# Kernel tuning notes

Measured on AMD Instinct MI355X. Metric: run time of the kernel, lower is better.

The kernel has to match this reference:

```python
import jax, jax.numpy as jnp
import numpy as np

L, B = 64, 7          # n_layers, n_bit_options
EPS = 0.02            # sinkhorn entropic regularizer
ITERS = 200           # sinkhorn iterations
TINY = 1e-40


def setup_inputs() -> dict:
    key = jax.random.key(0)
    k1, k2, k3, k4 = jax.random.split(key, 4)
    theta = jax.random.normal(k1, (L, B), dtype=jnp.float32)
    phi = jax.random.normal(k2, (B,), dtype=jnp.float32)
    # layer sizes (param counts), positive; matches layer_sizes buffer usage
    n = jax.random.uniform(k3, (L,), dtype=jnp.float32, minval=4096.0, maxval=262144.0)
    sens = jax.random.uniform(k4, (L,), dtype=jnp.float32)
    sens = sens / sens.sum()  # update_sensitivity normalizes to a distribution
    bits = jnp.arange(2, 2 + B, dtype=jnp.float32)
    err = 2.0 ** (-2.0 * bits)  # quantization error per bitwidth
    return {"theta": theta, "phi": phi, "n": n, "sens": sens, "err": err}


def reference(theta, phi, n, sens, err):
    # DiffAllocator.compute_P
    a = n / n.sum()                         # row marginal (buffer 'a')
    b = jax.nn.softmax(phi)                 # col marginal b()
    C = (n * sens)[:, None] * err[None, :]  # build_cost: [L,B]
    K = -(C - theta) / EPS                  # log-kernel
    log_a = jnp.log(a + TINY)
    log_b = jnp.log(b + TINY)
    f0 = jnp.zeros((L,), dtype=theta.dtype)
    g0 = jnp.zeros((B,), dtype=theta.dtype)

    def step(carry, _):
        f, g = carry
        f = log_a - jax.scipy.special.logsumexp(K + g[None, :], axis=1)
        g = log_b - jax.scipy.special.logsumexp(K + f[:, None], axis=0)
        return (f, g), None

    (f, g), _ = jax.lax.scan(step, (f0, g0), None, length=ITERS)
    P = jnp.exp(K + f[:, None] + g[None, :])
    return P / (P.sum() + TINY)
```

## Files before the change

### kernel.cpp

```cpp
#include <hip/hip_runtime.h>
#include <math.h>

#define NB 7
#define EPS_ 0.02f
#define ITERS1_ 120
#define ITERS2_ 80
#define TINY_ 1e-40f
#define LOG2E_ 1.4426950408889634f
#define LN2_   0.6931471805599453f

__device__ __forceinline__ float exp2_hw(float x) {
#if __has_builtin(__builtin_amdgcn_exp2f)
    return __builtin_amdgcn_exp2f(x);
#else
    return __expf(x * LN2_);
#endif
}
__device__ __forceinline__ float log2_hw(float x) {
#if __has_builtin(__builtin_amdgcn_logf)
    return __builtin_amdgcn_logf(x);
#else
    return __logf(x) * LOG2E_;
#endif
}
__device__ __forceinline__ float rcp_hw(float x) {
#if __has_builtin(__builtin_amdgcn_rcpf)
    return __builtin_amdgcn_rcpf(x);
#else
    return 1.0f / x;
#endif
}
__device__ __forceinline__ float ldexp_hw(float x, int e) {
#if __has_builtin(__builtin_amdgcn_ldexpf)
    return __builtin_amdgcn_ldexpf(x, e);
#else
    float r; asm("v_ldexp_f32 %0, %1, %2" : "=v"(r) : "v"(x), "v"(e)); return r;
#endif
}
__device__ __forceinline__ float frexp_mant_hw(float x) {
#if __has_builtin(__builtin_amdgcn_frexp_mantf)
    return __builtin_amdgcn_frexp_mantf(x);
#else
    float r; asm("v_frexp_mant_f32 %0, %1" : "=v"(r) : "v"(x)); return r;
#endif
}
__device__ __forceinline__ int frexp_exp_hw(float x) {
#if __has_builtin(__builtin_amdgcn_frexp_expf)
    return __builtin_amdgcn_frexp_expf(x);
#else
    int r; asm("v_frexp_exp_i32_f32 %0, %1" : "=v"(r) : "v"(x)); return r;
#endif
}

template <int CTRL>
__device__ __forceinline__ float dpp_ident(float identity, float x) {
    return __int_as_float(__builtin_amdgcn_update_dpp(
        __float_as_int(identity), __float_as_int(x), CTRL, 0xF, 0xF, false));
}
__device__ __forceinline__ float readlane63(float x) {
    return __int_as_float(__builtin_amdgcn_readlane(__float_as_int(x), 63));
}
__device__ __forceinline__ float wave_sum_bcast(float s) {
    s += dpp_ident<0x111>(0.f, s);
    s += dpp_ident<0x112>(0.f, s);
    s += dpp_ident<0x114>(0.f, s);
    s += dpp_ident<0x118>(0.f, s);
    s += dpp_ident<0x142>(0.f, s);
    s += dpp_ident<0x143>(0.f, s);
    return readlane63(s);
}

#define WAVE_MAXI7(v0,v1,v2,v3,v4,v5,v6, m0,m1,m2,m3,m4,m5,m6)               \
  {                                                                           \
    int r0,r1,r2,r3,r4,r5,r6;                                                 \
    asm("v_max_i32_dpp %0, %14, %14 row_shr:1 row_mask:0xf bank_mask:0xf\n\t" \
        "v_max_i32_dpp %1, %15, %15 row_shr:1 row_mask:0xf bank_mask:0xf\n\t" \
        "v_max_i32_dpp %2, %16, %16 row_shr:1 row_mask:0xf bank_mask:0xf\n\t" \
        "v_max_i32_dpp %3, %17, %17 row_shr:1 row_mask:0xf bank_mask:0xf\n\t" \
        "v_max_i32_dpp %4, %18, %18 row_shr:1 row_mask:0xf bank_mask:0xf\n\t" \
        "v_max_i32_dpp %5, %19, %19 row_shr:1 row_mask:0xf bank_mask:0xf\n\t" \
        "v_max_i32_dpp %6, %20, %20 row_shr:1 row_mask:0xf bank_mask:0xf\n\t" \
        "v_max_i32_dpp %0, %0, %0 row_shr:2 row_mask:0xf bank_mask:0xf\n\t"   \
        "v_max_i32_dpp %1, %1, %1 row_shr:2 row_mask:0xf bank_mask:0xf\n\t"   \
        "v_max_i32_dpp %2, %2, %2 row_shr:2 row_mask:0xf bank_mask:0xf\n\t"   \
        "v_max_i32_dpp %3, %3, %3 row_shr:2 row_mask:0xf bank_mask:0xf\n\t"   \
        "v_max_i32_dpp %4, %4, %4 row_shr:2 row_mask:0xf bank_mask:0xf\n\t"   \
        "v_max_i32_dpp %5, %5, %5 row_shr:2 row_mask:0xf bank_mask:0xf\n\t"   \
        "v_max_i32_dpp %6, %6, %6 row_shr:2 row_mask:0xf bank_mask:0xf\n\t"   \
        "v_max_i32_dpp %0, %0, %0 row_shr:4 row_mask:0xf bank_mask:0xf\n\t"   \
        "v_max_i32_dpp %1, %1, %1 row_shr:4 row_mask:0xf bank_mask:0xf\n\t"   \
        "v_max_i32_dpp %2, %2, %2 row_shr:4 row_mask:0xf bank_mask:0xf\n\t"   \
        "v_max_i32_dpp %3, %3, %3 row_shr:4 row_mask:0xf bank_mask:0xf\n\t"   \
        "v_max_i32_dpp %4, %4, %4 row_shr:4 row_mask:0xf bank_mask:0xf\n\t"   \
        "v_max_i32_dpp %5, %5, %5 row_shr:4 row_mask:0xf bank_mask:0xf\n\t"   \
        "v_max_i32_dpp %6, %6, %6 row_shr:4 row_mask:0xf bank_mask:0xf\n\t"   \
        "v_max_i32_dpp %0, %0, %0 row_shr:8 row_mask:0xf bank_mask:0xf\n\t"   \
        "v_max_i32_dpp %1, %1, %1 row_shr:8 row_mask:0xf bank_mask:0xf\n\t"   \
        "v_max_i32_dpp %2, %2, %2 row_shr:8 row_mask:0xf bank_mask:0xf\n\t"   \
        "v_max_i32_dpp %3, %3, %3 row_shr:8 row_mask:0xf bank_mask:0xf\n\t"   \
        "v_max_i32_dpp %4, %4, %4 row_shr:8 row_mask:0xf bank_mask:0xf\n\t"   \
        "v_max_i32_dpp %5, %5, %5 row_shr:8 row_mask:0xf bank_mask:0xf\n\t"   \
        "v_max_i32_dpp %6, %6, %6 row_shr:8 row_mask:0xf bank_mask:0xf\n\t"   \
        "v_max_i32_dpp %0, %0, %0 row_bcast:15 row_mask:0xa bank_mask:0xf\n\t"\
        "v_max_i32_dpp %1, %1, %1 row_bcast:15 row_mask:0xa bank_mask:0xf\n\t"\
        "v_max_i32_dpp %2, %2, %2 row_bcast:15 row_mask:0xa bank_mask:0xf\n\t"\
        "v_max_i32_dpp %3, %3, %3 row_bcast:15 row_mask:0xa bank_mask:0xf\n\t"\
        "v_max_i32_dpp %4, %4, %4 row_bcast:15 row_mask:0xa bank_mask:0xf\n\t"\
        "v_max_i32_dpp %5, %5, %5 row_bcast:15 row_mask:0xa bank_mask:0xf\n\t"\
        "v_max_i32_dpp %6, %6, %6 row_bcast:15 row_mask:0xa bank_mask:0xf\n\t"\
        "v_max_i32_dpp %0, %0, %0 row_bcast:31 row_mask:0xc bank_mask:0xf\n\t"\
        "v_max_i32_dpp %1, %1, %1 row_bcast:31 row_mask:0xc bank_mask:0xf\n\t"\
        "v_max_i32_dpp %2, %2, %2 row_bcast:31 row_mask:0xc bank_mask:0xf\n\t"\
        "v_max_i32_dpp %3, %3, %3 row_bcast:31 row_mask:0xc bank_mask:0xf\n\t"\
        "v_max_i32_dpp %4, %4, %4 row_bcast:31 row_mask:0xc bank_mask:0xf\n\t"\
        "v_max_i32_dpp %5, %5, %5 row_bcast:31 row_mask:0xc bank_mask:0xf\n\t"\
        "v_max_i32_dpp %6, %6, %6 row_bcast:31 row_mask:0xc bank_mask:0xf\n\t"\
        "v_readlane_b32 %7, %0, 63\n\t"                                       \
        "v_readlane_b32 %8, %1, 63\n\t"                                       \
        "v_readlane_b32 %9, %2, 63\n\t"                                       \
        "v_readlane_b32 %10, %3, 63\n\t"                                      \
        "v_readlane_b32 %11, %4, 63\n\t"                                      \
        "v_readlane_b32 %12, %5, 63\n\t"                                      \
        "v_readlane_b32 %13, %6, 63\n\t"                                      \
        "s_nop 1"                                                             \
        : "=&v"(r0), "=&v"(r1), "=&v"(r2), "=&v"(r3),                         \
          "=&v"(r4), "=&v"(r5), "=&v"(r6),                                    \
          "=s"(m0), "=s"(m1), "=s"(m2), "=s"(m3),                             \
          "=s"(m4), "=s"(m5), "=s"(m6)                                        \
        : "v"(v0), "v"(v1), "v"(v2), "v"(v3), "v"(v4), "v"(v5), "v"(v6));     \
  }

#define WAVE_SUM7(e0,e1,e2,e3,e4,e5,e6, s0_,s1_,s2_,s3_,s4_,s5_,s6_)          \
    asm("s_nop 1\n\t"                                                         \
        "v_add_f32_dpp %0, %0, %0 row_shr:1 row_mask:0xf bank_mask:0xf\n\t"   \
        "v_add_f32_dpp %1, %1, %1 row_shr:1 row_mask:0xf bank_mask:0xf\n\t"   \
        "v_add_f32_dpp %2, %2, %2 row_shr:1 row_mask:0xf bank_mask:0xf\n\t"   \
        "v_add_f32_dpp %3, %3, %3 row_shr:1 row_mask:0xf bank_mask:0xf\n\t"   \
        "v_add_f32_dpp %4, %4, %4 row_shr:1 row_mask:0xf bank_mask:0xf\n\t"   \
        "v_add_f32_dpp %5, %5, %5 row_shr:1 row_mask:0xf bank_mask:0xf\n\t"   \
        "v_add_f32_dpp %6, %6, %6 row_shr:1 row_mask:0xf bank_mask:0xf\n\t"   \
        "v_add_f32_dpp %0, %0, %0 row_shr:2 row_mask:0xf bank_mask:0xf\n\t"   \
        "v_add_f32_dpp %1, %1, %1 row_shr:2 row_mask:0xf bank_mask:0xf\n\t"   \
        "v_add_f32_dpp %2, %2, %2 row_shr:2 row_mask:0xf bank_mask:0xf\n\t"   \
        "v_add_f32_dpp %3, %3, %3 row_shr:2 row_mask:0xf bank_mask:0xf\n\t"   \
        "v_add_f32_dpp %4, %4, %4 row_shr:2 row_mask:0xf bank_mask:0xf\n\t"   \
        "v_add_f32_dpp %5, %5, %5 row_shr:2 row_mask:0xf bank_mask:0xf\n\t"   \
        "v_add_f32_dpp %6, %6, %6 row_shr:2 row_mask:0xf bank_mask:0xf\n\t"   \
        "v_add_f32_dpp %0, %0, %0 row_shr:4 row_mask:0xf bank_mask:0xf\n\t"   \
        "v_add_f32_dpp %1, %1, %1 row_shr:4 row_mask:0xf bank_mask:0xf\n\t"   \
        "v_add_f32_dpp %2, %2, %2 row_shr:4 row_mask:0xf bank_mask:0xf\n\t"   \
        "v_add_f32_dpp %3, %3, %3 row_shr:4 row_mask:0xf bank_mask:0xf\n\t"   \
        "v_add_f32_dpp %4, %4, %4 row_shr:4 row_mask:0xf bank_mask:0xf\n\t"   \
        "v_add_f32_dpp %5, %5, %5 row_shr:4 row_mask:0xf bank_mask:0xf\n\t"   \
        "v_add_f32_dpp %6, %6, %6 row_shr:4 row_mask:0xf bank_mask:0xf\n\t"   \
        "v_add_f32_dpp %0, %0, %0 row_shr:8 row_mask:0xf bank_mask:0xf\n\t"   \
        "v_add_f32_dpp %1, %1, %1 row_shr:8 row_mask:0xf bank_mask:0xf\n\t"   \
        "v_add_f32_dpp %2, %2, %2 row_shr:8 row_mask:0xf bank_mask:0xf\n\t"   \
        "v_add_f32_dpp %3, %3, %3 row_shr:8 row_mask:0xf bank_mask:0xf\n\t"   \
        "v_add_f32_dpp %4, %4, %4 row_shr:8 row_mask:0xf bank_mask:0xf\n\t"   \
        "v_add_f32_dpp %5, %5, %5 row_shr:8 row_mask:0xf bank_mask:0xf\n\t"   \
        "v_add_f32_dpp %6, %6, %6 row_shr:8 row_mask:0xf bank_mask:0xf\n\t"   \
        "v_add_f32_dpp %0, %0, %0 row_bcast:15 row_mask:0xa bank_mask:0xf\n\t"\
        "v_add_f32_dpp %1, %1, %1 row_bcast:15 row_mask:0xa bank_mask:0xf\n\t"\
        "v_add_f32_dpp %2, %2, %2 row_bcast:15 row_mask:0xa bank_mask:0xf\n\t"\
        "v_add_f32_dpp %3, %3, %3 row_bcast:15 row_mask:0xa bank_mask:0xf\n\t"\
        "v_add_f32_dpp %4, %4, %4 row_bcast:15 row_mask:0xa bank_mask:0xf\n\t"\
        "v_add_f32_dpp %5, %5, %5 row_bcast:15 row_mask:0xa bank_mask:0xf\n\t"\
        "v_add_f32_dpp %6, %6, %6 row_bcast:15 row_mask:0xa bank_mask:0xf\n\t"\
        "v_add_f32_dpp %0, %0, %0 row_bcast:31 row_mask:0xc bank_mask:0xf\n\t"\
        "v_add_f32_dpp %1, %1, %1 row_bcast:31 row_mask:0xc bank_mask:0xf\n\t"\
        "v_add_f32_dpp %2, %2, %2 row_bcast:31 row_mask:0xc bank_mask:0xf\n\t"\
        "v_add_f32_dpp %3, %3, %3 row_bcast:31 row_mask:0xc bank_mask:0xf\n\t"\
        "v_add_f32_dpp %4, %4, %4 row_bcast:31 row_mask:0xc bank_mask:0xf\n\t"\
        "v_add_f32_dpp %5, %5, %5 row_bcast:31 row_mask:0xc bank_mask:0xf\n\t"\
        "v_add_f32_dpp %6, %6, %6 row_bcast:31 row_mask:0xc bank_mask:0xf\n\t"\
        "v_readlane_b32 %7, %0, 63\n\t"                                       \
        "v_readlane_b32 %8, %1, 63\n\t"                                       \
        "v_readlane_b32 %9, %2, 63\n\t"                                       \
        "v_readlane_b32 %10, %3, 63\n\t"                                      \
        "v_readlane_b32 %11, %4, 63\n\t"                                      \
        "v_readlane_b32 %12, %5, 63\n\t"                                      \
        "v_readlane_b32 %13, %6, 63\n\t"                                      \
        "s_nop 1"                                                             \
        : "+v"(e0), "+v"(e1), "+v"(e2), "+v"(e3),                             \
          "+v"(e4), "+v"(e5), "+v"(e6),                                       \
          "=s"(s0_), "=s"(s1_), "=s"(s2_), "=s"(s3_),                         \
          "=s"(s4_), "=s"(s5_), "=s"(s6_))

#define WAVE_SUM7_SRC(w0,w1,w2,w3,w4,w5,w6, s0_,s1_,s2_,s3_,s4_,s5_,s6_)     \
  {                                                                           \
    float r0,r1,r2,r3,r4,r5,r6;                                               \
    asm("s_nop 1\n\t"                                                         \
        "v_add_f32_dpp %0, %14, %14 row_shr:1 row_mask:0xf bank_mask:0xf\n\t" \
        "v_add_f32_dpp %1, %15, %15 row_shr:1 row_mask:0xf bank_mask:0xf\n\t" \
        "v_add_f32_dpp %2, %16, %16 row_shr:1 row_mask:0xf bank_mask:0xf\n\t" \
        "v_add_f32_dpp %3, %17, %17 row_shr:1 row_mask:0xf bank_mask:0xf\n\t" \
        "v_add_f32_dpp %4, %18, %18 row_shr:1 row_mask:0xf bank_mask:0xf\n\t" \
        "v_add_f32_dpp %5, %19, %19 row_shr:1 row_mask:0xf bank_mask:0xf\n\t" \
        "v_add_f32_dpp %6, %20, %20 row_shr:1 row_mask:0xf bank_mask:0xf\n\t" \
        "v_add_f32_dpp %0, %0, %0 row_shr:2 row_mask:0xf bank_mask:0xf\n\t"   \
        "v_add_f32_dpp %1, %1, %1 row_shr:2 row_mask:0xf bank_mask:0xf\n\t"   \
        "v_add_f32_dpp %2, %2, %2 row_shr:2 row_mask:0xf bank_mask:0xf\n\t"   \
        "v_add_f32_dpp %3, %3, %3 row_shr:2 row_mask:0xf bank_mask:0xf\n\t"   \
        "v_add_f32_dpp %4, %4, %4 row_shr:2 row_mask:0xf bank_mask:0xf\n\t"   \
        "v_add_f32_dpp %5, %5, %5 row_shr:2 row_mask:0xf bank_mask:0xf\n\t"   \
        "v_add_f32_dpp %6, %6, %6 row_shr:2 row_mask:0xf bank_mask:0xf\n\t"   \
        "v_add_f32_dpp %0, %0, %0 row_shr:4 row_mask:0xf bank_mask:0xf\n\t"   \
        "v_add_f32_dpp %1, %1, %1 row_shr:4 row_mask:0xf bank_mask:0xf\n\t"   \
        "v_add_f32_dpp %2, %2, %2 row_shr:4 row_mask:0xf bank_mask:0xf\n\t"   \
        "v_add_f32_dpp %3, %3, %3 row_shr:4 row_mask:0xf bank_mask:0xf\n\t"   \
        "v_add_f32_dpp %4, %4, %4 row_shr:4 row_mask:0xf bank_mask:0xf\n\t"   \
        "v_add_f32_dpp %5, %5, %5 row_shr:4 row_mask:0xf bank_mask:0xf\n\t"   \
        "v_add_f32_dpp %6, %6, %6 row_shr:4 row_mask:0xf bank_mask:0xf\n\t"   \
        "v_add_f32_dpp %0, %0, %0 row_shr:8 row_mask:0xf bank_mask:0xf\n\t"   \
        "v_add_f32_dpp %1, %1, %1 row_shr:8 row_mask:0xf bank_mask:0xf\n\t"   \
        "v_add_f32_dpp %2, %2, %2 row_shr:8 row_mask:0xf bank_mask:0xf\n\t"   \
        "v_add_f32_dpp %3, %3, %3 row_shr:8 row_mask:0xf bank_mask:0xf\n\t"   \
        "v_add_f32_dpp %4, %4, %4 row_shr:8 row_mask:0xf bank_mask:0xf\n\t"   \
        "v_add_f32_dpp %5, %5, %5 row_shr:8 row_mask:0xf bank_mask:0xf\n\t"   \
        "v_add_f32_dpp %6, %6, %6 row_shr:8 row_mask:0xf bank_mask:0xf\n\t"   \
        "v_add_f32_dpp %0, %0, %0 row_bcast:15 row_mask:0xa bank_mask:0xf\n\t"\
        "v_add_f32_dpp %1, %1, %1 row_bcast:15 row_mask:0xa bank_mask:0xf\n\t"\
        "v_add_f32_dpp %2, %2, %2 row_bcast:15 row_mask:0xa bank_mask:0xf\n\t"\
        "v_add_f32_dpp %3, %3, %3 row_bcast:15 row_mask:0xa bank_mask:0xf\n\t"\
        "v_add_f32_dpp %4, %4, %4 row_bcast:15 row_mask:0xa bank_mask:0xf\n\t"\
        "v_add_f32_dpp %5, %5, %5 row_bcast:15 row_mask:0xa bank_mask:0xf\n\t"\
        "v_add_f32_dpp %6, %6, %6 row_bcast:15 row_mask:0xa bank_mask:0xf\n\t"\
        "v_add_f32_dpp %0, %0, %0 row_bcast:31 row_mask:0xc bank_mask:0xf\n\t"\
        "v_add_f32_dpp %1, %1, %1 row_bcast:31 row_mask:0xc bank_mask:0xf\n\t"\
        "v_add_f32_dpp %2, %2, %2 row_bcast:31 row_mask:0xc bank_mask:0xf\n\t"\
        "v_add_f32_dpp %3, %3, %3 row_bcast:31 row_mask:0xc bank_mask:0xf\n\t"\
        "v_add_f32_dpp %4, %4, %4 row_bcast:31 row_mask:0xc bank_mask:0xf\n\t"\
        "v_add_f32_dpp %5, %5, %5 row_bcast:31 row_mask:0xc bank_mask:0xf\n\t"\
        "v_add_f32_dpp %6, %6, %6 row_bcast:31 row_mask:0xc bank_mask:0xf\n\t"\
        "v_readlane_b32 %7, %0, 63\n\t"                                       \
        "v_readlane_b32 %8, %1, 63\n\t"                                       \
        "v_readlane_b32 %9, %2, 63\n\t"                                       \
        "v_readlane_b32 %10, %3, 63\n\t"                                      \
        "v_readlane_b32 %11, %4, 63\n\t"                                      \
        "v_readlane_b32 %12, %5, 63\n\t"                                      \
        "v_readlane_b32 %13, %6, 63\n\t"                                      \
        "s_nop 1"                                                             \
        : "=&v"(r0), "=&v"(r1), "=&v"(r2), "=&v"(r3),                         \
          "=&v"(r4), "=&v"(r5), "=&v"(r6),                                    \
          "=s"(s0_), "=s"(s1_), "=s"(s2_), "=s"(s3_),                         \
          "=s"(s4_), "=s"(s5_), "=s"(s6_)                                     \
        : "v"(w0), "v"(w1), "v"(w2), "v"(w3), "v"(w4), "v"(w5), "v"(w6));     \
  }

__global__ __launch_bounds__(64) void sinkhorn_kernel(
    const float* __restrict__ theta,
    const float* __restrict__ phi,
    const float* __restrict__ n,
    const float* __restrict__ sens,
    const float* __restrict__ err,
    float* __restrict__ out)
{
    const int lane = threadIdx.x;

    const float ni = n[lane];
    const float si = sens[lane];

    const float kscale = LOG2E_ / EPS_;
    float K2[NB];
    #pragma unroll
    for (int j = 0; j < NB; ++j)
        K2[j] = (theta[lane * NB + j] - ni * si * err[j]) * kscale;

    const float nsum   = wave_sum_bcast(ni);
    const float aT     = ni / nsum + TINY_;
    const float log_a2 = log2_hw(aT);

    float t2v[NB];
    #pragma unroll
    for (int j = 0; j < NB; ++j) t2v[j] = phi[j] * LOG2E_;
    float pmax = t2v[0];
    #pragma unroll
    for (int j = 1; j < NB; ++j) pmax = fmaxf(pmax, t2v[j]);
    float psum = 0.f;
    #pragma unroll
    for (int j = 0; j < NB; ++j) psum += exp2_hw(t2v[j] - pmax);
    const float lps = log2_hw(psum);
    float bT[NB], cb[NB];
    #pragma unroll
    for (int j = 0; j < NB; ++j) {
        bT[j]     = exp2_hw(t2v[j] - pmax - lps) + TINY_;
        const float log_b2 = log2_hw(bT[j]);
        cb[j]     = log_b2 - log_a2;
    }
    float b2c[NB], ibc[NB];
    #pragma unroll
    for (int j = 0; j < NB; ++j) {
        b2c[j] = exp2_hw(cb[j]);
        ibc[j] = exp2_hw(-cb[j]);
    }

    float Mm[NB]; int iE[NB];
    #pragma unroll
    for (int j = 0; j < NB; ++j) {
        const float y  = K2[j] - log_a2;
        const float yi = rintf(y);
        iE[j] = (int)yi;
        Mm[j] = exp2_hw(y - yi);
    }

    int XcS0 = 0, XcS1 = 0, XcS2 = 0, XcS3 = 0, XcS4 = 0, XcS5 = 0, XcS6 = 0;
    const unsigned SLO = 0x17800000u, SHI = 0x67800000u;

    for (int it = 0; it < ITERS1_; ++it) {
        const int X = max(max(max(iE[0], iE[1]), max(iE[2], iE[3])),
                          max(max(iE[4], iE[5]), iE[6]));
        const int xe0 = iE[0]-X, xe1 = iE[1]-X, xe2 = iE[2]-X, xe3 = iE[3]-X,
                  xe4 = iE[4]-X, xe5 = iE[5]-X, xe6 = iE[6]-X;
        const float f0 = ldexp_hw(Mm[0], xe0), f1 = ldexp_hw(Mm[1], xe1),
                    f2 = ldexp_hw(Mm[2], xe2), f3 = ldexp_hw(Mm[3], xe3),
                    f4 = ldexp_hw(Mm[4], xe4), f5 = ldexp_hw(Mm[5], xe5),
                    f6 = ldexp_hw(Mm[6], xe6);
        const float s  = ((f0 + f1) + (f2 + f3)) + ((f4 + f5) + f6);
        const float rs = rcp_hw(s);

        const float g0 = (Mm[0]*ibc[0])*rs, g1 = (Mm[1]*ibc[1])*rs,
                    g2 = (Mm[2]*ibc[2])*rs, g3 = (Mm[3]*ibc[3])*rs,
                    g4 = (Mm[4]*ibc[4])*rs, g5 = (Mm[5]*ibc[5])*rs,
                    g6 = (Mm[6]*ibc[6])*rs;

        int d0 = xe0-XcS0, d1 = xe1-XcS1, d2 = xe2-XcS2, d3 = xe3-XcS3,
            d4 = xe4-XcS4, d5 = xe5-XcS5, d6 = xe6-XcS6;
        float h0 = ldexp_hw(g0, d0), h1 = ldexp_hw(g1, d1),
              h2 = ldexp_hw(g2, d2), h3 = ldexp_hw(g3, d3),
              h4 = ldexp_hw(g4, d4), h5 = ldexp_hw(g5, d5),
              h6 = ldexp_hw(g6, d6);

        float ss0, ss1, ss2, ss3, ss4, ss5, ss6;
        WAVE_SUM7(h0, h1, h2, h3, h4, h5, h6,
                  ss0, ss1, ss2, ss3, ss4, ss5, ss6);

        const unsigned u0 = __float_as_uint(ss0), u1 = __float_as_uint(ss1),
                       u2 = __float_as_uint(ss2), u3 = __float_as_uint(ss3),
                       u4 = __float_as_uint(ss4), u5 = __float_as_uint(ss5),
                       u6 = __float_as_uint(ss6);
        const unsigned umin = min(min(min(u0, u1), min(u2, u3)),
                                  min(min(u4, u5), u6));
        const unsigned umax = max(max(max(u0, u1), max(u2, u3)),
                                  max(max(u4, u5), u6));
        if (umin < SLO || umax > SHI) {
            int C0, C1, C2, C3, C4, C5, C6;
            WAVE_MAXI7(xe0, xe1, xe2, xe3, xe4, xe5, xe6,
                       C0, C1, C2, C3, C4, C5, C6);
            d0 = xe0-C0; d1 = xe1-C1; d2 = xe2-C2; d3 = xe3-C3;
            d4 = xe4-C4; d5 = xe5-C5; d6 = xe6-C6;
            h0 = ldexp_hw(g0, d0); h1 = ldexp_hw(g1, d1);
            h2 = ldexp_hw(g2, d2); h3 = ldexp_hw(g3, d3);
            h4 = ldexp_hw(g4, d4); h5 = ldexp_hw(g5, d5);
            h6 = ldexp_hw(g6, d6);
            WAVE_SUM7(h0, h1, h2, h3, h4, h5, h6,
                      ss0, ss1, ss2, ss3, ss4, ss5, ss6);
            XcS0 = C0; XcS1 = C1; XcS2 = C2; XcS3 = C3;
            XcS4 = C4; XcS5 = C5; XcS6 = C6;
        }

        const float r0 = rcp_hw(ss0), r1 = rcp_hw(ss1), r2 = rcp_hw(ss2),
                    r3 = rcp_hw(ss3), r4 = rcp_hw(ss4), r5 = rcp_hw(ss5),
                    r6 = rcp_hw(ss6);
        const float w0 = (g0*r0)*b2c[0], w1 = (g1*r1)*b2c[1],
                    w2 = (g2*r2)*b2c[2], w3 = (g3*r3)*b2c[3],
                    w4 = (g4*r4)*b2c[4], w5 = (g5*r5)*b2c[5],
                    w6 = (g6*r6)*b2c[6];
        Mm[0] = frexp_mant_hw(w0); iE[0] = frexp_exp_hw(w0) + d0;
        Mm[1] = frexp_mant_hw(w1); iE[1] = frexp_exp_hw(w1) + d1;
        Mm[2] = frexp_mant_hw(w2); iE[2] = frexp_exp_hw(w2) + d2;
        Mm[3] = frexp_mant_hw(w3); iE[3] = frexp_exp_hw(w3) + d3;
        Mm[4] = frexp_mant_hw(w4); iE[4] = frexp_exp_hw(w4) + d4;
        Mm[5] = frexp_mant_hw(w5); iE[5] = frexp_exp_hw(w5) + d5;
        Mm[6] = frexp_mant_hw(w6); iE[6] = frexp_exp_hw(w6) + d6;
    }

    float U[NB], B[NB];
    #pragma unroll
    for (int j = 0; j < NB; ++j) {
        U[j] = ldexp_hw(Mm[j] * ibc[j], iE[j]);
        B[j] = b2c[j];
    }

    for (int it = 0; it < ITERS2_; ++it) {
        float p0 = U[0] * B[0], p1 = U[1] * B[1], p2 = U[2] * B[2],
              p3 = U[3] * B[3], p4 = U[4] * B[4], p5 = U[5] * B[5],
              p6 = U[6] * B[6];
        const float s = ((p0 + p1) + (p2 + p3)) + ((p4 + p5) + p6);
        const float rs = rcp_hw(s);
        float w0 = U[0] * rs, w1 = U[1] * rs, w2 = U[2] * rs,
              w3 = U[3] * rs, w4 = U[4] * rs, w5 = U[5] * rs,
              w6 = U[6] * rs;

        float ss0, ss1, ss2, ss3, ss4, ss5, ss6;
        WAVE_SUM7_SRC(w0, w1, w2, w3, w4, w5, w6,
                      ss0, ss1, ss2, ss3, ss4, ss5, ss6);

        const float r0 = rcp_hw(ss0);
        const float r1 = rcp_hw(ss1);
        const float r2 = rcp_hw(ss2);
        const float r3 = rcp_hw(ss3);
        const float r4 = rcp_hw(ss4);
        const float r5 = rcp_hw(ss5);
        const float r6 = rcp_hw(ss6);
        U[0] = w0 * r0; U[1] = w1 * r1; U[2] = w2 * r2; U[3] = w3 * r3;
        U[4] = w4 * r4; U[5] = w5 * r5; U[6] = w6 * r6;
    }

    float pr[NB];
    float rowsum = 0.f;
    #pragma unroll
    for (int j = 0; j < NB; ++j) {
        pr[j] = U[j] * bT[j];
        rowsum += pr[j];
    }
    const float total = wave_sum_bcast(rowsum);
    const float inv = 1.0f / (total + TINY_);
    #pragma unroll
    for (int j = 0; j < NB; ++j)
        out[lane * NB + j] = pr[j] * inv;
}

extern "C" void kernel_launch(void* const* d_in, const int* in_sizes, int n_in,
                              void* d_out, int out_size, void* d_ws, size_t ws_size,
                              hipStream_t stream) {
    const float* theta = (const float*)d_in[0];
    const float* phi   = (const float*)d_in[1];
    const float* n     = (const float*)d_in[2];
    const float* sens  = (const float*)d_in[3];
    const float* err   = (const float*)d_in[4];
    float* out = (float*)d_out;

    sinkhorn_kernel<<<1, 64, 0, stream>>>(theta, phi, n, sens, err, out);
}
```

Before: 113.8 us.

## Add frozen-exponent fast path for early Sinkhorn phase iterations

Phase 1 of the Sinkhorn loop used to renormalise exponents with frexp and ldexp on every iteration. It now does that only every PERIOD_ iterations, after an initial FULLN_ full iterations. In between it freezes a per-row and per-column power-of-two frame (RA/CA) and runs plain float multiplies, with wave-wide range checks that drop back to the full path on overflow or underflow risk. This removes the ldexp and frexp work from most iterations, but adds ballot and branch overhead plus possible retries, and it relies on the frozen frame staying within range.

```diff
diff --git a/kernel.cpp b/kernel.cpp
--- a/kernel.cpp
+++ b/kernel.cpp
@@ -5,6 +5,8 @@
 #define EPS_ 0.02f
 #define ITERS1_ 120
 #define ITERS2_ 80
+#define FULLN_  16
+#define PERIOD_ 16
 #define TINY_ 1e-40f
 #define LOG2E_ 1.4426950408889634f
 #define LN2_   0.6931471805599453f
@@ -50,6 +52,15 @@
 #else
     int r; asm("v_frexp_exp_i32_f32 %0, %1" : "=v"(r) : "v"(x)); return r;
 #endif
+}
+__device__ __forceinline__ float mant_of(float w) {
+    return __int_as_float((__float_as_int(w) & 0x007fffff) | 0x3f800000);
+}
+__device__ __forceinline__ int exp_of(float w) {
+    return ((__float_as_int(w) >> 23) & 0xff) - 127;
+}
+__device__ __forceinline__ float exp2i_nonpos(int e) {
+    return (e >= -126) ? __int_as_float((e + 127) << 23) : 0.0f;
 }
 
 template <int CTRL>
@@ -295,94 +306,165 @@
         ibc[j] = exp2_hw(-cb[j]);
     }
 
-    float Mm[NB]; int iE[NB];
+    float v[NB]; int Fe[NB];
     #pragma unroll
     for (int j = 0; j < NB; ++j) {
         const float y  = K2[j] - log_a2;
         const float yi = rintf(y);
-        iE[j] = (int)yi;
-        Mm[j] = exp2_hw(y - yi);
+        Fe[j] = (int)yi;
+        v[j]  = exp2_hw(y - yi);
     }
 
     int XcS0 = 0, XcS1 = 0, XcS2 = 0, XcS3 = 0, XcS4 = 0, XcS5 = 0, XcS6 = 0;
-    const unsigned SLO = 0x17800000u, SHI = 0x67800000u;
-
-    for (int it = 0; it < ITERS1_; ++it) {
-        const int X = max(max(max(iE[0], iE[1]), max(iE[2], iE[3])),
-                          max(max(iE[4], iE[5]), iE[6]));
-        const int xe0 = iE[0]-X, xe1 = iE[1]-X, xe2 = iE[2]-X, xe3 = iE[3]-X,
-                  xe4 = iE[4]-X, xe5 = iE[5]-X, xe6 = iE[6]-X;
-        const float f0 = ldexp_hw(Mm[0], xe0), f1 = ldexp_hw(Mm[1], xe1),
-                    f2 = ldexp_hw(Mm[2], xe2), f3 = ldexp_hw(Mm[3], xe3),
-                    f4 = ldexp_hw(Mm[4], xe4), f5 = ldexp_hw(Mm[5], xe5),
-                    f6 = ldexp_hw(Mm[6], xe6);
-        const float s  = ((f0 + f1) + (f2 + f3)) + ((f4 + f5) + f6);
-        const float rs = rcp_hw(s);
-
-        const float g0 = (Mm[0]*ibc[0])*rs, g1 = (Mm[1]*ibc[1])*rs,
-                    g2 = (Mm[2]*ibc[2])*rs, g3 = (Mm[3]*ibc[3])*rs,
-                    g4 = (Mm[4]*ibc[4])*rs, g5 = (Mm[5]*ibc[5])*rs,
-                    g6 = (Mm[6]*ibc[6])*rs;
-
-        int d0 = xe0-XcS0, d1 = xe1-XcS1, d2 = xe2-XcS2, d3 = xe3-XcS3,
-            d4 = xe4-XcS4, d5 = xe5-XcS5, d6 = xe6-XcS6;
-        float h0 = ldexp_hw(g0, d0), h1 = ldexp_hw(g1, d1),
-              h2 = ldexp_hw(g2, d2), h3 = ldexp_hw(g3, d3),
-              h4 = ldexp_hw(g4, d4), h5 = ldexp_hw(g5, d5),
-              h6 = ldexp_hw(g6, d6);
-
-        float ss0, ss1, ss2, ss3, ss4, ss5, ss6;
-        WAVE_SUM7(h0, h1, h2, h3, h4, h5, h6,
-                  ss0, ss1, ss2, ss3, ss4, ss5, ss6);
-
-        const unsigned u0 = __float_as_uint(ss0), u1 = __float_as_uint(ss1),
-                       u2 = __float_as_uint(ss2), u3 = __float_as_uint(ss3),
-                       u4 = __float_as_uint(ss4), u5 = __float_as_uint(ss5),
-                       u6 = __float_as_uint(ss6);
-        const unsigned umin = min(min(min(u0, u1), min(u2, u3)),
-                                  min(min(u4, u5), u6));
-        const unsigned umax = max(max(max(u0, u1), max(u2, u3)),
-                                  max(max(u4, u5), u6));
-        if (umin < SLO || umax > SHI) {
-            int C0, C1, C2, C3, C4, C5, C6;
-            WAVE_MAXI7(xe0, xe1, xe2, xe3, xe4, xe5, xe6,
-                       C0, C1, C2, C3, C4, C5, C6);
-            d0 = xe0-C0; d1 = xe1-C1; d2 = xe2-C2; d3 = xe3-C3;
-            d4 = xe4-C4; d5 = xe5-C5; d6 = xe6-C6;
-            h0 = ldexp_hw(g0, d0); h1 = ldexp_hw(g1, d1);
-            h2 = ldexp_hw(g2, d2); h3 = ldexp_hw(g3, d3);
-            h4 = ldexp_hw(g4, d4); h5 = ldexp_hw(g5, d5);
-            h6 = ldexp_hw(g6, d6);
+    float RA[NB], CA[NB];
+    bool have_frame = false;
+    int since = 0;
+
+    const unsigned LO80 = 0x17800000u, HI80 = 0x67800000u;
+    const float SLOf = __int_as_float(0x33800000);
+    const float SHIf = __int_as_float(0x4b800000);
+    const unsigned TLO = 0x26800000u, THI = 0x58800000u;
+
+    int it = 0;
+    while (it < ITERS1_) {
+        if (have_frame && it >= FULLN_ && since < PERIOD_) {
+            const float f0 = v[0]*RA[0], f1 = v[1]*RA[1], f2 = v[2]*RA[2],
+                        f3 = v[3]*RA[3], f4 = v[4]*RA[4], f5 = v[5]*RA[5],
+                        f6 = v[6]*RA[6];
+            const float s = ((f0 + f1) + (f2 + f3)) + ((f4 + f5) + f6);
+            const bool ok = (s >= SLOf) && (s <= SHIf);
+            if (__ballot(ok) != ~0ull) { have_frame = false; continue; }
+            const float rs = rcp_hw(s);
+            const float g0 = (v[0]*ibc[0])*rs, g1 = (v[1]*ibc[1])*rs,
+                        g2 = (v[2]*ibc[2])*rs, g3 = (v[3]*ibc[3])*rs,
+                        g4 = (v[4]*ibc[4])*rs, g5 = (v[5]*ibc[5])*rs,
+                        g6 = (v[6]*ibc[6])*rs;
+            float h0 = g0*CA[0], h1 = g1*CA[1], h2 = g2*CA[2], h3 = g3*CA[3],
+                  h4 = g4*CA[4], h5 = g5*CA[5], h6 = g6*CA[6];
+            float T0, T1, T2, T3, T4, T5, T6;
+            WAVE_SUM7(h0, h1, h2, h3, h4, h5, h6, T0, T1, T2, T3, T4, T5, T6);
+            const unsigned u0 = __float_as_uint(T0), u1 = __float_as_uint(T1),
+                           u2 = __float_as_uint(T2), u3 = __float_as_uint(T3),
+                           u4 = __float_as_uint(T4), u5 = __float_as_uint(T5),
+                           u6 = __float_as_uint(T6);
+            const unsigned umin = min(min(min(u0, u1), min(u2, u3)),
+                                      min(min(u4, u5), u6));
+            const unsigned umax = max(max(max(u0, u1), max(u2, u3)),
+                                      max(max(u4, u5), u6));
+            if (umin < TLO || umax > THI) { have_frame = false; continue; }
+            const float r0 = rcp_hw(T0), r1 = rcp_hw(T1), r2 = rcp_hw(T2),
+                        r3 = rcp_hw(T3), r4 = rcp_hw(T4), r5 = rcp_hw(T5),
+                        r6 = rcp_hw(T6);
+            v[0] = (g0*r0)*b2c[0]; v[1] = (g1*r1)*b2c[1];
+            v[2] = (g2*r2)*b2c[2]; v[3] = (g3*r3)*b2c[3];
+            v[4] = (g4*r4)*b2c[4]; v[5] = (g5*r5)*b2c[5];
+            v[6] = (g6*r6)*b2c[6];
+            ++since; ++it; continue;
+        }
+
+        #pragma unroll
+        for (int j = 0; j < NB; ++j) {
+            Fe[j] += exp_of(v[j]);
+            v[j]   = mant_of(v[j]);
+        }
+
+        {
+            const int X = max(max(max(Fe[0], Fe[1]), max(Fe[2], Fe[3])),
+                              max(max(Fe[4], Fe[5]), Fe[6]));
+            const int xe0 = Fe[0]-X, xe1 = Fe[1]-X, xe2 = Fe[2]-X,
+                      xe3 = Fe[3]-X, xe4 = Fe[4]-X, xe5 = Fe[5]-X,
+                      xe6 = Fe[6]-X;
+            const float f0 = ldexp_hw(v[0], xe0), f1 = ldexp_hw(v[1], xe1),
+                        f2 = ldexp_hw(v[2], xe2), f3 = ldexp_hw(v[3], xe3),
+                        f4 = ldexp_hw(v[4], xe4), f5 = ldexp_hw(v[5], xe5),
+                        f6 = ldexp_hw(v[6], xe6);
+            const float s  = ((f0 + f1) + (f2 + f3)) + ((f4 + f5) + f6);
+            const float rs = rcp_hw(s);
+
+            const float g0 = (v[0]*ibc[0])*rs, g1 = (v[1]*ibc[1])*rs,
+                        g2 = (v[2]*ibc[2])*rs, g3 = (v[3]*ibc[3])*rs,
+                        g4 = (v[4]*ibc[4])*rs, g5 = (v[5]*ibc[5])*rs,
+                        g6 = (v[6]*ibc[6])*rs;
+
+            int d0 = xe0-XcS0, d1 = xe1-XcS1, d2 = xe2-XcS2, d3 = xe3-XcS3,
+                d4 = xe4-XcS4, d5 = xe5-XcS5, d6 = xe6-XcS6;
+            float h0 = ldexp_hw(g0, d0), h1 = ldexp_hw(g1, d1),
+                  h2 = ldexp_hw(g2, d2), h3 = ldexp_hw(g3, d3),
+                  h4 = ldexp_hw(g4, d4), h5 = ldexp_hw(g5, d5),
+                  h6 = ldexp_hw(g6, d6);
+
+            float ss0, ss1, ss2, ss3, ss4, ss5, ss6;
             WAVE_SUM7(h0, h1, h2, h3, h4, h5, h6,
                       ss0, ss1, ss2, ss3, ss4, ss5, ss6);
-            XcS0 = C0; XcS1 = C1; XcS2 = C2; XcS3 = C3;
-            XcS4 = C4; XcS5 = C5; XcS6 = C6;
+
+            const unsigned u0 = __float_as_uint(ss0), u1 = __float_as_uint(ss1),
+                           u2 = __float_as_uint(ss2), u3 = __float_as_uint(ss3),
+                           u4 = __float_as_uint(ss4), u5 = __float_as_uint(ss5),
+                           u6 = __float_as_uint(ss6);
+            const unsigned umin = min(min(min(u0, u1), min(u2, u3)),
+                                      min(min(u4, u5), u6));
+            const unsigned umax = max(max(max(u0, u1), max(u2, u3)),
+                                      max(max(u4, u5), u6));
+            if (umin < LO80 || umax > HI80) {
+                int C0, C1, C2, C3, C4, C5, C6;
+                WAVE_MAXI7(xe0, xe1, xe2, xe3, xe4, xe5, xe6,
+                           C0, C1, C2, C3, C4, C5, C6);
+                d0 = xe0-C0; d1 = xe1-C1; d2 = xe2-C2; d3 = xe3-C3;
+                d4 = xe4-C4; d5 = xe5-C5; d6 = xe6-C6;
+                h0 = ldexp_hw(g0, d0); h1 = ldexp_hw(g1, d1);
+                h2 = ldexp_hw(g2, d2); h3 = ldexp_hw(g3, d3);
+                h4 = ldexp_hw(g4, d4); h5 = ldexp_hw(g5, d5);
+                h6 = ldexp_hw(g6, d6);
+                WAVE_SUM7(h0, h1, h2, h3, h4, h5, h6,
+                          ss0, ss1, ss2, ss3, ss4, ss5, ss6);
+                XcS0 = C0; XcS1 = C1; XcS2 = C2; XcS3 = C3;
+                XcS4 = C4; XcS5 = C5; XcS6 = C6;
+            }
+
+            const float r0 = rcp_hw(ss0), r1 = rcp_hw(ss1), r2 = rcp_hw(ss2),
+                        r3 = rcp_hw(ss3), r4 = rcp_hw(ss4), r5 = rcp_hw(ss5),
+                        r6 = rcp_hw(ss6);
+            const float w0 = (g0*r0)*b2c[0], w1 = (g1*r1)*b2c[1],
+                        w2 = (g2*r2)*b2c[2], w3 = (g3*r3)*b2c[3],
+                        w4 = (g4*r4)*b2c[4], w5 = (g5*r5)*b2c[5],
+                        w6 = (g6*r6)*b2c[6];
+            v[0] = frexp_mant_hw(w0); Fe[0] = frexp_exp_hw(w0) + d0;
+            v[1] = frexp_mant_hw(w1); Fe[1] = frexp_exp_hw(w1) + d1;
+            v[2] = frexp_mant_hw(w2); Fe[2] = frexp_exp_hw(w2) + d2;
+            v[3] = frexp_mant_hw(w3); Fe[3] = frexp_exp_hw(w3) + d3;
+            v[4] = frexp_mant_hw(w4); Fe[4] = frexp_exp_hw(w4) + d4;
+            v[5] = frexp_mant_hw(w5); Fe[5] = frexp_exp_hw(w5) + d5;
+            v[6] = frexp_mant_hw(w6); Fe[6] = frexp_exp_hw(w6) + d6;
         }
 
-        const float r0 = rcp_hw(ss0), r1 = rcp_hw(ss1), r2 = rcp_hw(ss2),
-                    r3 = rcp_hw(ss3), r4 = rcp_hw(ss4), r5 = rcp_hw(ss5),
-                    r6 = rcp_hw(ss6);
-        const float w0 = (g0*r0)*b2c[0], w1 = (g1*r1)*b2c[1],
-                    w2 = (g2*r2)*b2c[2], w3 = (g3*r3)*b2c[3],
-                    w4 = (g4*r4)*b2c[4], w5 = (g5*r5)*b2c[5],
-                    w6 = (g6*r6)*b2c[6];
-        Mm[0] = frexp_mant_hw(w0); iE[0] = frexp_exp_hw(w0) + d0;
-        Mm[1] = frexp_mant_hw(w1); iE[1] = frexp_exp_hw(w1) + d1;
-        Mm[2] = frexp_mant_hw(w2); iE[2] = frexp_exp_hw(w2) + d2;
-        Mm[3] = frexp_mant_hw(w3); iE[3] = frexp_exp_hw(w3) + d3;
-        Mm[4] = frexp_mant_hw(w4); iE[4] = frexp_exp_hw(w4) + d4;
-        Mm[5] = frexp_mant_hw(w5); iE[5] = frexp_exp_hw(w5) + d5;
-        Mm[6] = frexp_mant_hw(w6); iE[6] = frexp_exp_hw(w6) + d6;
+        if (it + 1 >= FULLN_ && it + 1 < ITERS1_) {
+            const int X2 = max(max(max(Fe[0], Fe[1]), max(Fe[2], Fe[3])),
+                               max(max(Fe[4], Fe[5]), Fe[6]));
+            const int y0 = Fe[0]-X2, y1 = Fe[1]-X2, y2 = Fe[2]-X2,
+                      y3 = Fe[3]-X2, y4 = Fe[4]-X2, y5 = Fe[5]-X2,
+                      y6 = Fe[6]-X2;
+            WAVE_MAXI7(y0, y1, y2, y3, y4, y5, y6,
+                       XcS0, XcS1, XcS2, XcS3, XcS4, XcS5, XcS6);
+            RA[0] = exp2i_nonpos(y0); CA[0] = exp2i_nonpos(y0 - XcS0);
+            RA[1] = exp2i_nonpos(y1); CA[1] = exp2i_nonpos(y1 - XcS1);
+            RA[2] = exp2i_nonpos(y2); CA[2] = exp2i_nonpos(y2 - XcS2);
+            RA[3] = exp2i_nonpos(y3); CA[3] = exp2i_nonpos(y3 - XcS3);
+            RA[4] = exp2i_nonpos(y4); CA[4] = exp2i_nonpos(y4 - XcS4);
+            RA[5] = exp2i_nonpos(y5); CA[5] = exp2i_nonpos(y5 - XcS5);
+            RA[6] = exp2i_nonpos(y6); CA[6] = exp2i_nonpos(y6 - XcS6);
+            have_frame = true;
+        }
+        since = 0; ++it;
     }
 
     float U[NB], B[NB];
     #pragma unroll
     for (int j = 0; j < NB; ++j) {
-        U[j] = ldexp_hw(Mm[j] * ibc[j], iE[j]);
+        U[j] = ldexp_hw(v[j] * ibc[j], Fe[j]);
         B[j] = b2c[j];
     }
 
-    for (int it = 0; it < ITERS2_; ++it) {
+    for (int it2 = 0; it2 < ITERS2_; ++it2) {
         float p0 = U[0] * B[0], p1 = U[1] * B[1], p2 = U[2] * B[2],
               p3 = U[3] * B[3], p4 = U[4] * B[4], p5 = U[5] * B[5],
               p6 = U[6] * B[6];
```

Result: slower. 126.9 us (+11.5%).
